# Optimization experiments

Measured on AMD Instinct MI355X. Metric: run time of the kernel, lower is better.

The kernel has to match this reference:

```python
import jax, jax.numpy as jnp
import numpy as np

START_IDX = 1
STOP_IDX = 2
VOCAB = 32000
EMB = 512
HID = 512


def setup_inputs() -> dict:
    key = jax.random.key(0)
    ks = jax.random.split(key, 10)
    B, T = 64, 50
    x = jax.random.normal(ks[0], (B, HID), dtype=jnp.float32)
    labels = jax.random.randint(ks[1], (B, T), 0, VOCAB, dtype=jnp.int64)
    s = 0.02
    emb = jax.random.normal(ks[2], (VOCAB, EMB), dtype=jnp.float32) * s
    W_ih = jax.random.normal(ks[3], (4 * HID, EMB), dtype=jnp.float32) * s
    W_hh = jax.random.normal(ks[4], (4 * HID, HID), dtype=jnp.float32) * s
    b_ih = jax.random.normal(ks[5], (4 * HID,), dtype=jnp.float32) * s
    b_hh = jax.random.normal(ks[6], (4 * HID,), dtype=jnp.float32) * s
    fc_W = jax.random.normal(ks[7], (VOCAB, HID), dtype=jnp.float32) * s
    fc_b = jax.random.normal(ks[8], (VOCAB,), dtype=jnp.float32) * s
    return {"x": x, "labels": labels, "emb": emb, "W_ih": W_ih, "W_hh": W_hh,
            "b_ih": b_ih, "b_hh": b_hh, "fc_W": fc_W, "fc_b": fc_b}


def _decode_loss(x, labels, emb, W_ih, W_hh, b_ih, b_hh, fc_W, fc_b):
    B, T = labels.shape
    # teacher-forced inputs: [START, y_0..y_{T-1}]; targets: [y_0..y_{T-1}, STOP]
    inputs = jnp.concatenate([jnp.full((B, 1), START_IDX, labels.dtype), labels], axis=1)
    targets = jnp.concatenate([labels, jnp.full((B, 1), STOP_IDX, labels.dtype)], axis=1)
    x_emb = emb[inputs]                       # [B, T+1, E]
    x_emb_t = jnp.swapaxes(x_emb, 0, 1)       # [T+1, B, E]

    def step(carry, xt):
        h, c = carry
        gates = xt @ W_ih.T + b_ih + h @ W_hh.T + b_hh   # [B, 4H]
        i, f, g, o = jnp.split(gates, 4, axis=-1)         # torch gate order i,f,g,o
        i = jax.nn.sigmoid(i); f = jax.nn.sigmoid(f)
        g = jnp.tanh(g); o = jax.nn.sigmoid(o)
        c = f * c + i * g
        h = o * jnp.tanh(c)
        return (h, c), h

    # init_states(x[i]): hidden and cell initialized from image feature
    (_, _), hs = jax.lax.scan(step, (x, x), x_emb_t)      # hs: [T+1, B, H]
    logits = hs @ fc_W.T + fc_b                            # [T+1, B, V]
    logp = jax.nn.log_softmax(logits, axis=-1)
    tgt = jnp.swapaxes(targets, 0, 1)[..., None]           # [T+1, B, 1]
    nll = -jnp.take_along_axis(logp, tgt, axis=-1)         # [T+1, B, 1]
    # original: per-step CrossEntropyLoss on batch of 1, summed over steps, / batch_size
    return nll.sum() / B


def reference(x, labels, emb, W_ih, W_hh, b_ih, b_hh, fc_W, fc_b):
    return _decode_loss(x, labels, emb, W_ih, W_hh, b_ih, b_hh, fc_W, fc_b)
```

## Files before the change

### kernel.cpp

```cpp
#include <hip/hip_runtime.h>
#include <cstddef>
#include <cstdint>

#define B_  64
#define T_  51
#define H_  512
#define G4_ 2048
#define V_  32000
#define R_  (T_ * B_)

typedef __attribute__((ext_vector_type(8))) short bf16x8;
typedef __attribute__((ext_vector_type(4))) float f32x4;
typedef __attribute__((ext_vector_type(4))) unsigned int u32x4;
typedef unsigned long long ull;

__device__ __forceinline__ uint16_t f2bf(float f) {
    uint32_t u = __float_as_uint(f);
    u += 0x7FFFu + ((u >> 16) & 1u);
    return (uint16_t)(u >> 16);
}
__device__ __forceinline__ float bf2f(uint32_t h) { return __uint_as_float(h << 16); }

__device__ __forceinline__ void ldsc(u32x4& d, const uint32_t* p) {
    asm volatile("global_load_dwordx4 %0, %1, off sc0 sc1" : "=v"(d) : "v"(p));
}
__device__ __forceinline__ uint32_t ldflag(const uint32_t* p) {
    uint32_t v;
    asm volatile("global_load_dword %0, %1, off sc0 sc1\n\ts_waitcnt vmcnt(0)"
                 : "=v"(v) : "v"(p));
    return v;
}
__device__ __forceinline__ void stflag(uint32_t* p, uint32_t v) {
    asm volatile("global_store_dword %0, %1, off sc0 sc1" :: "v"(p), "v"(v) : "memory");
}
__device__ __forceinline__ void stsh(uint16_t* p, uint32_t v) {
    asm volatile("global_store_short %0, %1, off sc0 sc1" :: "v"(p), "v"(v) : "memory");
}

__device__ __forceinline__ void gl_lds16(const void* g, void* l) {
    __builtin_amdgcn_global_load_lds((const __attribute__((address_space(1))) void*)g,
                                     (__attribute__((address_space(3))) void*)l, 16, 0, 0);
}

__global__ __launch_bounds__(256) void k0_init(const float* __restrict__ x,
                                               uint16_t* __restrict__ hx,
                                               float* __restrict__ sumexp,
                                               uint32_t* __restrict__ flags) {
    int i = blockIdx.x * 256 + threadIdx.x;
    if (i < B_ * H_) hx[i] = f2bf(x[i]);
    if (i < R_) sumexp[i] = 0.f;
    if (i < T_ * 128) flags[i] = 0;
}

__global__ __launch_bounds__(256) void kcvt(const float* __restrict__ src,
                                            uint16_t* __restrict__ dst, int n8) {
    int i = blockIdx.x * 256 + threadIdx.x;
    if (i >= n8) return;
    const float4* s = (const float4*)src + (size_t)i * 2;
    float4 f0 = s[0], f1 = s[1];
    union { uint16_t h[8]; uint4 u; } p;
    p.h[0]=f2bf(f0.x); p.h[1]=f2bf(f0.y); p.h[2]=f2bf(f0.z); p.h[3]=f2bf(f0.w);
    p.h[4]=f2bf(f1.x); p.h[5]=f2bf(f1.y); p.h[6]=f2bf(f1.z); p.h[7]=f2bf(f1.w);
    ((uint4*)dst)[i] = p.u;
}

template<int CVT>
__global__ __launch_bounds__(256, 2) void k1_mfma(const int* __restrict__ labels,
                                                  const float* __restrict__ emb,
                                                  const void* __restrict__ wih,
                                                  const float* __restrict__ b_ih,
                                                  const float* __restrict__ b_hh,
                                                  uint16_t* __restrict__ XgT) {
    __shared__ uint16_t Al[64 * 72];
    __shared__ uint16_t Bl[256 * 72];
    const int t    = blockIdx.y;
    const int n0   = blockIdx.x * 256;
    const int tid  = threadIdx.x;
    const int w    = tid >> 6;
    const int lane = tid & 63;
    const int l15  = lane & 15;
    const int lhi  = lane >> 4;

    f32x4 acc[4][4];
    #pragma unroll
    for (int mi = 0; mi < 4; ++mi)
        #pragma unroll
        for (int nf = 0; nf < 4; ++nf) acc[mi][nf] = (f32x4){0.f, 0.f, 0.f, 0.f};

    for (int k0 = 0; k0 < H_; k0 += 64) {
        #pragma unroll
        for (int r = 0; r < 2; ++r) {
            int idx = r * 256 + tid, row = idx >> 3, seg = idx & 7;
            int tok = (t == 0) ? 1 : labels[row * 50 + (t - 1)];
            const float* s = emb + (size_t)tok * H_ + k0 + seg * 8;
            float4 f0 = *(const float4*)s;
            float4 f1 = *(const float4*)(s + 4);
            union { uint16_t h[8]; uint4 u; } p;
            p.h[0]=f2bf(f0.x); p.h[1]=f2bf(f0.y); p.h[2]=f2bf(f0.z); p.h[3]=f2bf(f0.w);
            p.h[4]=f2bf(f1.x); p.h[5]=f2bf(f1.y); p.h[6]=f2bf(f1.z); p.h[7]=f2bf(f1.w);
            *(uint4*)(Al + row * 72 + seg * 8) = p.u;
        }
        #pragma unroll
        for (int r = 0; r < 8; ++r) {
            int idx = r * 256 + tid, row = idx >> 3, seg = idx & 7;
            if (CVT) {
                const float* s = (const float*)wih + (size_t)(n0 + row) * H_ + k0 + seg * 8;
                float4 f0 = *(const float4*)s;
                float4 f1 = *(const float4*)(s + 4);
                union { uint16_t h[8]; uint4 u; } p;
                p.h[0]=f2bf(f0.x); p.h[1]=f2bf(f0.y); p.h[2]=f2bf(f0.z); p.h[3]=f2bf(f0.w);
                p.h[4]=f2bf(f1.x); p.h[5]=f2bf(f1.y); p.h[6]=f2bf(f1.z); p.h[7]=f2bf(f1.w);
                *(uint4*)(Bl + row * 72 + seg * 8) = p.u;
            } else {
                *(uint4*)(Bl + row * 72 + seg * 8) =
                    *(const uint4*)((const uint16_t*)wih + (size_t)(n0 + row) * H_ + k0 + seg * 8);
            }
        }
        __syncthreads();
        #pragma unroll
        for (int ks = 0; ks < 2; ++ks) {
            bf16x8 a[4];
            #pragma unroll
            for (int mi = 0; mi < 4; ++mi)
                a[mi] = *(const bf16x8*)(Al + (mi * 16 + l15) * 72 + ks * 32 + lhi * 8);
            #pragma unroll
            for (int nf = 0; nf < 4; ++nf) {
                bf16x8 b = *(const bf16x8*)(Bl + (w * 64 + nf * 16 + l15) * 72 + ks * 32 + lhi * 8);
                #pragma unroll
                for (int mi = 0; mi < 4; ++mi)
                    acc[mi][nf] = __builtin_amdgcn_mfma_f32_16x16x32_bf16(a[mi], b, acc[mi][nf], 0, 0, 0);
            }
        }
        __syncthreads();
    }
    float bias[4];
    #pragma unroll
    for (int nf = 0; nf < 4; ++nf) {
        int col = n0 + w * 64 + nf * 16 + l15;
        bias[nf] = b_ih[col] + b_hh[col];
    }
    #pragma unroll
    for (int mi = 0; mi < 4; ++mi)
        #pragma unroll
        for (int nf = 0; nf < 4; ++nf) {
            const int col = n0 + w * 64 + nf * 16 + l15;
            const int g = col >> 9, u = col & 511;
            const int b = mi * 16 + lhi * 4;
            union { uint16_t h[4]; ull q; } pk;
            #pragma unroll
            for (int q = 0; q < 4; ++q) pk.h[q] = f2bf(acc[mi][nf][q] + bias[nf]);
            *(ull*)(XgT + ((size_t)(t * 512 + u) * 4 + g) * 64 + b) = pk.q;
        }
}

__global__ __launch_bounds__(256, 1) void k2p(const uint16_t* __restrict__ hx,
                                              const float* __restrict__ x,
                                              const uint16_t* __restrict__ XgT,
                                              const float* __restrict__ W_hh,
                                              uint16_t* __restrict__ hs,
                                              uint32_t* __restrict__ flags) {
    __shared__ uint16_t Wl[64 * 520];
    const int tid  = threadIdx.x;
    const int bid  = blockIdx.x;
    const int u0   = bid * 16;
    const int w    = tid >> 6;
    const int lane = tid & 63;
    const int l15  = lane & 15;
    const int lhi  = lane >> 4;
    const int arow = w * 16 + l15;

    {
        const int c = tid >> 2;
        const int q = tid & 3;
        const int j = (c >> 4) * 512 + u0 + (c & 15);
        const float* src = W_hh + (size_t)j * H_ + q * 128;
        uint16_t* dst = Wl + c * 520 + q * 128;
        #pragma unroll
        for (int i = 0; i < 128; i += 8) {
            float4 f0 = *(const float4*)(src + i);
            float4 f1 = *(const float4*)(src + i + 4);
            union { uint16_t h[8]; uint4 u; } p;
            p.h[0]=f2bf(f0.x); p.h[1]=f2bf(f0.y); p.h[2]=f2bf(f0.z); p.h[3]=f2bf(f0.w);
            p.h[4]=f2bf(f1.x); p.h[5]=f2bf(f1.y); p.h[6]=f2bf(f1.z); p.h[7]=f2bf(f1.w);
            *(uint4*)(dst + i) = p.u;
        }
    }
    float cst[4];
    #pragma unroll
    for (int q = 0; q < 4; ++q)
        cst[q] = x[(size_t)(w * 16 + lhi * 4 + q) * H_ + u0 + l15];
    __syncthreads();

    for (int t = 0; t < T_; ++t) {
        ull xgp[4];
        #pragma unroll
        for (int g = 0; g < 4; ++g)
            xgp[g] = *(const ull*)(XgT + ((size_t)(t * 512 + u0 + l15) * 4 + g) * 64 + w * 16 + lhi * 4);

        u32x4 ha[16];
        if (t == 0) {
            const uint16_t* hb = hx + (size_t)arow * H_ + lhi * 8;
            #pragma unroll
            for (int ks = 0; ks < 16; ++ks)
                ha[ks] = *(const u32x4*)(hb + ks * 32);
        } else {
            const uint32_t* fp = flags + (size_t)(t - 1) * 128 + (lane & 31) * 4 + w;
            for (;;) {
                uint32_t fv = 1;
                if (lane < 32) fv = ldflag(fp);
                if (!__any((int)(fv == 0))) break;
            }
            __builtin_amdgcn_sched_barrier(0);
            const uint16_t* hb = hs + ((size_t)(t - 1) * 64 + arow) * H_ + lhi * 8;
            #pragma unroll
            for (int ks = 0; ks < 16; ++ks)
                ldsc(ha[ks], (const uint32_t*)(hb + ks * 32));
        }
        f32x4 acc[4];
        #pragma unroll
        for (int nf = 0; nf < 4; ++nf) acc[nf] = (f32x4){0.f, 0.f, 0.f, 0.f};
        if (t != 0) { asm volatile("s_waitcnt vmcnt(8)" ::: "memory");
                      __builtin_amdgcn_sched_barrier(0); }
        #pragma unroll
        for (int ks = 0; ks < 8; ++ks) {
            union { u32x4 u; bf16x8 v; } au; au.u = ha[ks];
            #pragma unroll
            for (int nf = 0; nf < 4; ++nf) {
                bf16x8 b = *(const bf16x8*)(Wl + (nf * 16 + l15) * 520 + ks * 32 + lhi * 8);
                acc[nf] = __builtin_amdgcn_mfma_f32_16x16x32_bf16(au.v, b, acc[nf], 0, 0, 0);
            }
        }
        if (t != 0) { asm volatile("s_waitcnt vmcnt(0)" ::: "memory");
                      __builtin_amdgcn_sched_barrier(0); }
        #pragma unroll
        for (int ks = 8; ks < 16; ++ks) {
            union { u32x4 u; bf16x8 v; } au; au.u = ha[ks];
            #pragma unroll
            for (int nf = 0; nf < 4; ++nf) {
                bf16x8 b = *(const bf16x8*)(Wl + (nf * 16 + l15) * 520 + ks * 32 + lhi * 8);
                acc[nf] = __builtin_amdgcn_mfma_f32_16x16x32_bf16(au.v, b, acc[nf], 0, 0, 0);
            }
        }
        #pragma unroll
        for (int q = 0; q < 4; ++q) {
            const int b = w * 16 + lhi * 4 + q;
            float gi = acc[0][q] + bf2f((uint32_t)((xgp[0] >> (16 * q)) & 0xFFFF));
            float gf = acc[1][q] + bf2f((uint32_t)((xgp[1] >> (16 * q)) & 0xFFFF));
            float gg = acc[2][q] + bf2f((uint32_t)((xgp[2] >> (16 * q)) & 0xFFFF));
            float go = acc[3][q] + bf2f((uint32_t)((xgp[3] >> (16 * q)) & 0xFFFF));
            float si = 1.f / (1.f + __expf(-gi));
            float sf = 1.f / (1.f + __expf(-gf));
            float tg = tanhf(gg);
            float so = 1.f / (1.f + __expf(-go));
            float cc = sf * cst[q] + si * tg;
            cst[q] = cc;
            stsh(hs + (size_t)(t * 64 + b) * H_ + u0 + l15, (uint32_t)f2bf(so * tanhf(cc)));
        }
        asm volatile("s_waitcnt vmcnt(0)" ::: "memory");
        if (lane == 0) stflag(flags + (size_t)t * 128 + bid * 4 + w, (uint32_t)(t + 1));
    }
}

template<int CVT>
__global__ __launch_bounds__(512, 4) void k3_mfma(const uint16_t* __restrict__ hsb,
                                                  const void* __restrict__ fcw,
                                                  const float* __restrict__ fc_b,
                                                  const int* __restrict__ labels,
                                                  float* __restrict__ sumexp,
                                                  float* __restrict__ tgtlog) {
    __shared__ uint16_t Al[128 * 64];
    __shared__ uint16_t Bl[256 * 64];
    const int flat = blockIdx.x;
    const int xcd  = flat & 7;
    const int slot = flat >> 3;
    const int work = (xcd < 2 ? xcd * 407 : 814 + (xcd - 2) * 406) + slot;
    const int m0   = (work % 26) * 128;
    const int v0   = (work / 26) * 256;
    const int tid  = threadIdx.x;
    const int w    = tid >> 6;
    const int lane = tid & 63;
    const int l15  = lane & 15;
    const int lhi  = lane >> 4;
    const int wm   = w >> 2;
    const int wn   = w & 3;

    f32x4 acc[4][4];
    #pragma unroll
    for (int mi = 0; mi < 4; ++mi)
        #pragma unroll
        for (int nf = 0; nf < 4; ++nf) acc[mi][nf] = (f32x4){0.f, 0.f, 0.f, 0.f};

    const int lrow = lane >> 3;
    const int segp = (lane & 7) ^ lrow;

    for (int k0 = 0; k0 < H_; k0 += 64) {
        #pragma unroll
        for (int r = 0; r < 2; ++r) {
            const int g = w * 2 + r, row0 = g * 8;
            int grow = m0 + row0 + lrow; if (grow >= R_) grow = R_ - 1;
            gl_lds16(hsb + (size_t)grow * H_ + k0 + segp * 8, Al + row0 * 64);
        }
        if (CVT == 0) {
            #pragma unroll
            for (int r = 0; r < 4; ++r) {
                const int g = w * 4 + r, row0 = g * 8;
                gl_lds16((const uint16_t*)fcw + (size_t)(v0 + row0 + lrow) * H_ + k0 + segp * 8,
                         Bl + row0 * 64);
            }
        } else {
            #pragma unroll
            for (int r = 0; r < 4; ++r) {
                int idx = r * 512 + tid, row = idx >> 3, seg = idx & 7;
                const float* s = (const float*)fcw + (size_t)(v0 + row) * H_ + k0 + seg * 8;
                float4 f0 = *(const float4*)s;
                float4 f1 = *(const float4*)(s + 4);
                union { uint16_t h[8]; uint4 u; } p;
                p.h[0]=f2bf(f0.x); p.h[1]=f2bf(f0.y); p.h[2]=f2bf(f0.z); p.h[3]=f2bf(f0.w);
                p.h[4]=f2bf(f1.x); p.h[5]=f2bf(f1.y); p.h[6]=f2bf(f1.z); p.h[7]=f2bf(f1.w);
                *(uint4*)(Bl + row * 64 + (seg ^ (row & 7)) * 8) = p.u;
            }
        }
        __syncthreads();
        #pragma unroll
        for (int ks = 0; ks < 2; ++ks) {
            bf16x8 a[4];
            #pragma unroll
            for (int mi = 0; mi < 4; ++mi) {
                const int ar = wm * 64 + mi * 16 + l15;
                a[mi] = *(const bf16x8*)((const char*)Al + ar * 128 +
                        ((ks * 64 + lhi * 16) ^ ((ar & 7) << 4)));
            }
            #pragma unroll
            for (int nf = 0; nf < 4; ++nf) {
                const int br = wn * 64 + nf * 16 + l15;
                bf16x8 b = *(const bf16x8*)((const char*)Bl + br * 128 +
                           ((ks * 64 + lhi * 16) ^ ((br & 7) << 4)));
                #pragma unroll
                for (int mi = 0; mi < 4; ++mi)
                    acc[mi][nf] = __builtin_amdgcn_mfma_f32_16x16x32_bf16(a[mi], b, acc[mi][nf], 0, 0, 0);
            }
        }
        __syncthreads();
    }
    float bias[4];
    #pragma unroll
    for (int nf = 0; nf < 4; ++nf) bias[nf] = fc_b[v0 + wn * 64 + nf * 16 + l15];
    #pragma unroll
    for (int mi = 0; mi < 4; ++mi) {
        #pragma unroll
        for (int q = 0; q < 4; ++q) {
            const int r = m0 + wm * 64 + mi * 16 + lhi * 4 + q;
            if (r >= R_) continue;
            const int t = r >> 6, b = r & 63;
            const int tgt = (t < 50) ? labels[b * 50 + t] : 2;
            float lsum = 0.f;
            #pragma unroll
            for (int nf = 0; nf < 4; ++nf) {
                const int v = v0 + wn * 64 + nf * 16 + l15;
                float lg = acc[mi][nf][q] + bias[nf];
                lsum += __expf(lg);
                if (v == tgt) tgtlog[r] = lg;
            }
            lsum += __shfl_xor(lsum, 1, 16);
            lsum += __shfl_xor(lsum, 2, 16);
            lsum += __shfl_xor(lsum, 4, 16);
            lsum += __shfl_xor(lsum, 8, 16);
            if (l15 == 0) atomicAdd(&sumexp[r], lsum);
        }
    }
}

__global__ __launch_bounds__(256) void k4_loss(const float* __restrict__ sumexp,
                                               const float* __restrict__ tgtlog,
                                               float* __restrict__ out) {
    __shared__ float red[256];
    float s = 0.f;
    for (int r = threadIdx.x; r < R_; r += 256) s += logf(sumexp[r]) - tgtlog[r];
    red[threadIdx.x] = s;
    __syncthreads();
    for (int st = 128; st > 0; st >>= 1) {
        if (threadIdx.x < st) red[threadIdx.x] += red[threadIdx.x + st];
        __syncthreads();
    }
    if (threadIdx.x == 0) out[0] = red[0] / 64.0f;
}

extern "C" void kernel_launch(void* const* d_in, const int* in_sizes, int n_in,
                              void* d_out, int out_size, void* d_ws, size_t ws_size,
                              hipStream_t stream) {
    const float* x      = (const float*)d_in[0];
    const int*   labels = (const int*)d_in[1];
    const float* emb    = (const float*)d_in[2];
    const float* W_ih   = (const float*)d_in[3];
    const float* W_hh   = (const float*)d_in[4];
    const float* b_ih   = (const float*)d_in[5];
    const float* b_hh   = (const float*)d_in[6];
    const float* fc_W   = (const float*)d_in[7];
    const float* fc_b   = (const float*)d_in[8];
    float* out = (float*)d_out;

    char* p = (char*)d_ws;
    uint16_t* XgT    = (uint16_t*)p;  p += (size_t)T_ * 512 * 4 * 64 * 2;
    uint16_t* hsb    = (uint16_t*)p;  p += (size_t)R_ * H_ * 2;
    uint16_t* hx     = (uint16_t*)p;  p += (size_t)B_ * H_ * 2;
    float*    sumexp = (float*)p;     p += (size_t)R_ * 4;
    float*    tgtl   = (float*)p;     p += (size_t)R_ * 4;
    uint32_t* flags  = (uint32_t*)p;  p += (size_t)T_ * 128 * 4 + 256;
    uint16_t* fcwb   = (uint16_t*)p;  p += (size_t)V_ * H_ * 2;
    uint16_t* wihb   = (uint16_t*)p;  p += (size_t)G4_ * H_ * 2;
    const bool pre = ((size_t)(p - (char*)d_ws) <= ws_size);

    k0_init<<<128, 256, 0, stream>>>(x, hx, sumexp, flags);
    if (pre) {
        kcvt<<<8000, 256, 0, stream>>>(fc_W, fcwb, (V_ * H_) / 8);
        kcvt<<<512, 256, 0, stream>>>(W_ih, wihb, (G4_ * H_) / 8);
        k1_mfma<0><<<dim3(8, 51), 256, 0, stream>>>(labels, emb, wihb, b_ih, b_hh, XgT);
    } else {
        k1_mfma<1><<<dim3(8, 51), 256, 0, stream>>>(labels, emb, W_ih, b_ih, b_hh, XgT);
    }
    k2p<<<32, 256, 0, stream>>>(hx, x, XgT, W_hh, hsb, flags);
    if (pre) k3_mfma<0><<<3250, 512, 0, stream>>>(hsb, fcwb, fc_b, labels, sumexp, tgtl);
    else     k3_mfma<1><<<3250, 512, 0, stream>>>(hsb, fc_W, fc_b, labels, sumexp, tgtl);
    k4_loss<<<1, 256, 0, stream>>>(sumexp, tgtl, out);
}
```

Before: 508.3 us.

## Fuse LSTM recurrence and vocab projection into one persistent kernel with flag-based overlap

Merges the recurrent kernel and the vocabulary-projection/softmax kernel into one launch of 256 blocks. The first 32 blocks run the LSTM recurrence while the other 224 blocks loop over 128x256 output tiles, each spinning on per-timestep flags until the hidden states it needs exist. The point is to overlap the latency-bound serial recurrence with the large projection GEMM. In exchange the GEMM path drops the async global-to-LDS loads and the XOR swizzle in favour of register-staged padded LDS with atomic loads, and its grid shrinks from 3250 blocks of 512 threads to 224 persistent blocks of 256 threads. This may cut GEMM throughput, and correctness depends on all blocks being co-resident.

```diff
diff --git a/kernel.cpp b/kernel.cpp
--- a/kernel.cpp
+++ b/kernel.cpp
@@ -8,6 +8,8 @@
 #define G4_ 2048
 #define V_  32000
 #define R_  (T_ * B_)
+#define NTILE 3250
+#define NFC   224
 
 typedef __attribute__((ext_vector_type(8))) short bf16x8;
 typedef __attribute__((ext_vector_type(4))) float f32x4;
@@ -35,11 +37,6 @@
 }
 __device__ __forceinline__ void stsh(uint16_t* p, uint32_t v) {
     asm volatile("global_store_short %0, %1, off sc0 sc1" :: "v"(p), "v"(v) : "memory");
-}
-
-__device__ __forceinline__ void gl_lds16(const void* g, void* l) {
-    __builtin_amdgcn_global_load_lds((const __attribute__((address_space(1))) void*)g,
-                                     (__attribute__((address_space(3))) void*)l, 16, 0, 0);
 }
 
 __global__ __launch_bounds__(256) void k0_init(const float* __restrict__ x,
@@ -153,220 +150,216 @@
         }
 }
 
-__global__ __launch_bounds__(256, 1) void k2p(const uint16_t* __restrict__ hx,
-                                              const float* __restrict__ x,
-                                              const uint16_t* __restrict__ XgT,
-                                              const float* __restrict__ W_hh,
-                                              uint16_t* __restrict__ hs,
-                                              uint32_t* __restrict__ flags) {
-    __shared__ uint16_t Wl[64 * 520];
-    const int tid  = threadIdx.x;
+template<int CVT>
+__global__ __launch_bounds__(256) void k23(const uint16_t* __restrict__ hx,
+                                           const float* __restrict__ x,
+                                           const uint16_t* __restrict__ XgT,
+                                           const float* __restrict__ W_hh,
+                                           uint16_t* __restrict__ hs,
+                                           uint32_t* __restrict__ flags,
+                                           const void* __restrict__ fcw,
+                                           const float* __restrict__ fc_b,
+                                           const int* __restrict__ labels,
+                                           float* __restrict__ sumexp,
+                                           float* __restrict__ tgtlog) {
+    __shared__ uint16_t smem[64 * 520];
     const int bid  = blockIdx.x;
-    const int u0   = bid * 16;
-    const int w    = tid >> 6;
-    const int lane = tid & 63;
-    const int l15  = lane & 15;
-    const int lhi  = lane >> 4;
-    const int arow = w * 16 + l15;
-
-    {
-        const int c = tid >> 2;
-        const int q = tid & 3;
-        const int j = (c >> 4) * 512 + u0 + (c & 15);
-        const float* src = W_hh + (size_t)j * H_ + q * 128;
-        uint16_t* dst = Wl + c * 520 + q * 128;
-        #pragma unroll
-        for (int i = 0; i < 128; i += 8) {
-            float4 f0 = *(const float4*)(src + i);
-            float4 f1 = *(const float4*)(src + i + 4);
-            union { uint16_t h[8]; uint4 u; } p;
-            p.h[0]=f2bf(f0.x); p.h[1]=f2bf(f0.y); p.h[2]=f2bf(f0.z); p.h[3]=f2bf(f0.w);
-            p.h[4]=f2bf(f1.x); p.h[5]=f2bf(f1.y); p.h[6]=f2bf(f1.z); p.h[7]=f2bf(f1.w);
-            *(uint4*)(dst + i) = p.u;
-        }
-    }
-    float cst[4];
-    #pragma unroll
-    for (int q = 0; q < 4; ++q)
-        cst[q] = x[(size_t)(w * 16 + lhi * 4 + q) * H_ + u0 + l15];
-    __syncthreads();
-
-    for (int t = 0; t < T_; ++t) {
-        ull xgp[4];
-        #pragma unroll
-        for (int g = 0; g < 4; ++g)
-            xgp[g] = *(const ull*)(XgT + ((size_t)(t * 512 + u0 + l15) * 4 + g) * 64 + w * 16 + lhi * 4);
-
-        u32x4 ha[16];
-        if (t == 0) {
-            const uint16_t* hb = hx + (size_t)arow * H_ + lhi * 8;
-            #pragma unroll
-            for (int ks = 0; ks < 16; ++ks)
-                ha[ks] = *(const u32x4*)(hb + ks * 32);
-        } else {
-            const uint32_t* fp = flags + (size_t)(t - 1) * 128 + (lane & 31) * 4 + w;
-            for (;;) {
-                uint32_t fv = 1;
-                if (lane < 32) fv = ldflag(fp);
-                if (!__any((int)(fv == 0))) break;
-            }
-            __builtin_amdgcn_sched_barrier(0);
-            const uint16_t* hb = hs + ((size_t)(t - 1) * 64 + arow) * H_ + lhi * 8;
-            #pragma unroll
-            for (int ks = 0; ks < 16; ++ks)
-                ldsc(ha[ks], (const uint32_t*)(hb + ks * 32));
-        }
-        f32x4 acc[4];
-        #pragma unroll
-        for (int nf = 0; nf < 4; ++nf) acc[nf] = (f32x4){0.f, 0.f, 0.f, 0.f};
-        if (t != 0) { asm volatile("s_waitcnt vmcnt(8)" ::: "memory");
-                      __builtin_amdgcn_sched_barrier(0); }
-        #pragma unroll
-        for (int ks = 0; ks < 8; ++ks) {
-            union { u32x4 u; bf16x8 v; } au; au.u = ha[ks];
-            #pragma unroll
-            for (int nf = 0; nf < 4; ++nf) {
-                bf16x8 b = *(const bf16x8*)(Wl + (nf * 16 + l15) * 520 + ks * 32 + lhi * 8);
-                acc[nf] = __builtin_amdgcn_mfma_f32_16x16x32_bf16(au.v, b, acc[nf], 0, 0, 0);
-            }
-        }
-        if (t != 0) { asm volatile("s_waitcnt vmcnt(0)" ::: "memory");
-                      __builtin_amdgcn_sched_barrier(0); }
-        #pragma unroll
-        for (int ks = 8; ks < 16; ++ks) {
-            union { u32x4 u; bf16x8 v; } au; au.u = ha[ks];
-            #pragma unroll
-            for (int nf = 0; nf < 4; ++nf) {
-                bf16x8 b = *(const bf16x8*)(Wl + (nf * 16 + l15) * 520 + ks * 32 + lhi * 8);
-                acc[nf] = __builtin_amdgcn_mfma_f32_16x16x32_bf16(au.v, b, acc[nf], 0, 0, 0);
-            }
-        }
-        #pragma unroll
-        for (int q = 0; q < 4; ++q) {
-            const int b = w * 16 + lhi * 4 + q;
-            float gi = acc[0][q] + bf2f((uint32_t)((xgp[0] >> (16 * q)) & 0xFFFF));
-            float gf = acc[1][q] + bf2f((uint32_t)((xgp[1] >> (16 * q)) & 0xFFFF));
-            float gg = acc[2][q] + bf2f((uint32_t)((xgp[2] >> (16 * q)) & 0xFFFF));
-            float go = acc[3][q] + bf2f((uint32_t)((xgp[3] >> (16 * q)) & 0xFFFF));
-            float si = 1.f / (1.f + __expf(-gi));
-            float sf = 1.f / (1.f + __expf(-gf));
-            float tg = tanhf(gg);
-            float so = 1.f / (1.f + __expf(-go));
-            float cc = sf * cst[q] + si * tg;
-            cst[q] = cc;
-            stsh(hs + (size_t)(t * 64 + b) * H_ + u0 + l15, (uint32_t)f2bf(so * tanhf(cc)));
-        }
-        asm volatile("s_waitcnt vmcnt(0)" ::: "memory");
-        if (lane == 0) stflag(flags + (size_t)t * 128 + bid * 4 + w, (uint32_t)(t + 1));
-    }
-}
-
-template<int CVT>
-__global__ __launch_bounds__(512, 4) void k3_mfma(const uint16_t* __restrict__ hsb,
-                                                  const void* __restrict__ fcw,
-                                                  const float* __restrict__ fc_b,
-                                                  const int* __restrict__ labels,
-                                                  float* __restrict__ sumexp,
-                                                  float* __restrict__ tgtlog) {
-    __shared__ uint16_t Al[128 * 64];
-    __shared__ uint16_t Bl[256 * 64];
-    const int flat = blockIdx.x;
-    const int xcd  = flat & 7;
-    const int slot = flat >> 3;
-    const int work = (xcd < 2 ? xcd * 407 : 814 + (xcd - 2) * 406) + slot;
-    const int m0   = (work % 26) * 128;
-    const int v0   = (work / 26) * 256;
     const int tid  = threadIdx.x;
     const int w    = tid >> 6;
     const int lane = tid & 63;
     const int l15  = lane & 15;
     const int lhi  = lane >> 4;
-    const int wm   = w >> 2;
-    const int wn   = w & 3;
-
-    f32x4 acc[4][4];
-    #pragma unroll
-    for (int mi = 0; mi < 4; ++mi)
-        #pragma unroll
-        for (int nf = 0; nf < 4; ++nf) acc[mi][nf] = (f32x4){0.f, 0.f, 0.f, 0.f};
-
-    const int lrow = lane >> 3;
-    const int segp = (lane & 7) ^ lrow;
-
-    for (int k0 = 0; k0 < H_; k0 += 64) {
-        #pragma unroll
-        for (int r = 0; r < 2; ++r) {
-            const int g = w * 2 + r, row0 = g * 8;
-            int grow = m0 + row0 + lrow; if (grow >= R_) grow = R_ - 1;
-            gl_lds16(hsb + (size_t)grow * H_ + k0 + segp * 8, Al + row0 * 64);
-        }
-        if (CVT == 0) {
-            #pragma unroll
-            for (int r = 0; r < 4; ++r) {
-                const int g = w * 4 + r, row0 = g * 8;
-                gl_lds16((const uint16_t*)fcw + (size_t)(v0 + row0 + lrow) * H_ + k0 + segp * 8,
-                         Bl + row0 * 64);
-            }
-        } else {
-            #pragma unroll
-            for (int r = 0; r < 4; ++r) {
-                int idx = r * 512 + tid, row = idx >> 3, seg = idx & 7;
-                const float* s = (const float*)fcw + (size_t)(v0 + row) * H_ + k0 + seg * 8;
-                float4 f0 = *(const float4*)s;
-                float4 f1 = *(const float4*)(s + 4);
+
+    if (bid < 32) {
+        uint16_t* Wl = smem;
+        const int u0   = bid * 16;
+        const int arow = w * 16 + l15;
+        {
+            const int c = tid >> 2;
+            const int q = tid & 3;
+            const int j = (c >> 4) * 512 + u0 + (c & 15);
+            const float* src = W_hh + (size_t)j * H_ + q * 128;
+            uint16_t* dst = Wl + c * 520 + q * 128;
+            #pragma unroll
+            for (int i = 0; i < 128; i += 8) {
+                float4 f0 = *(const float4*)(src + i);
+                float4 f1 = *(const float4*)(src + i + 4);
                 union { uint16_t h[8]; uint4 u; } p;
                 p.h[0]=f2bf(f0.x); p.h[1]=f2bf(f0.y); p.h[2]=f2bf(f0.z); p.h[3]=f2bf(f0.w);
                 p.h[4]=f2bf(f1.x); p.h[5]=f2bf(f1.y); p.h[6]=f2bf(f1.z); p.h[7]=f2bf(f1.w);
-                *(uint4*)(Bl + row * 64 + (seg ^ (row & 7)) * 8) = p.u;
-            }
-        }
-        __syncthreads();
-        #pragma unroll
-        for (int ks = 0; ks < 2; ++ks) {
-            bf16x8 a[4];
-            #pragma unroll
-            for (int mi = 0; mi < 4; ++mi) {
-                const int ar = wm * 64 + mi * 16 + l15;
-                a[mi] = *(const bf16x8*)((const char*)Al + ar * 128 +
-                        ((ks * 64 + lhi * 16) ^ ((ar & 7) << 4)));
-            }
-            #pragma unroll
-            for (int nf = 0; nf < 4; ++nf) {
-                const int br = wn * 64 + nf * 16 + l15;
-                bf16x8 b = *(const bf16x8*)((const char*)Bl + br * 128 +
-                           ((ks * 64 + lhi * 16) ^ ((br & 7) << 4)));
-                #pragma unroll
-                for (int mi = 0; mi < 4; ++mi)
-                    acc[mi][nf] = __builtin_amdgcn_mfma_f32_16x16x32_bf16(a[mi], b, acc[mi][nf], 0, 0, 0);
-            }
-        }
-        __syncthreads();
-    }
-    float bias[4];
-    #pragma unroll
-    for (int nf = 0; nf < 4; ++nf) bias[nf] = fc_b[v0 + wn * 64 + nf * 16 + l15];
-    #pragma unroll
-    for (int mi = 0; mi < 4; ++mi) {
-        #pragma unroll
-        for (int q = 0; q < 4; ++q) {
-            const int r = m0 + wm * 64 + mi * 16 + lhi * 4 + q;
-            if (r >= R_) continue;
-            const int t = r >> 6, b = r & 63;
-            const int tgt = (t < 50) ? labels[b * 50 + t] : 2;
-            float lsum = 0.f;
-            #pragma unroll
-            for (int nf = 0; nf < 4; ++nf) {
-                const int v = v0 + wn * 64 + nf * 16 + l15;
-                float lg = acc[mi][nf][q] + bias[nf];
-                lsum += __expf(lg);
-                if (v == tgt) tgtlog[r] = lg;
-            }
-            lsum += __shfl_xor(lsum, 1, 16);
-            lsum += __shfl_xor(lsum, 2, 16);
-            lsum += __shfl_xor(lsum, 4, 16);
-            lsum += __shfl_xor(lsum, 8, 16);
-            if (l15 == 0) atomicAdd(&sumexp[r], lsum);
-        }
+                *(uint4*)(dst + i) = p.u;
+            }
+        }
+        float cst[4];
+        #pragma unroll
+        for (int q = 0; q < 4; ++q)
+            cst[q] = x[(size_t)(w * 16 + lhi * 4 + q) * H_ + u0 + l15];
+        __syncthreads();
+
+        for (int t = 0; t < T_; ++t) {
+            ull xgp[4];
+            #pragma unroll
+            for (int g = 0; g < 4; ++g)
+                xgp[g] = *(const ull*)(XgT + ((size_t)(t * 512 + u0 + l15) * 4 + g) * 64 + w * 16 + lhi * 4);
+
+            u32x4 ha[16];
+            if (t == 0) {
+                const uint16_t* hb = hx + (size_t)arow * H_ + lhi * 8;
+                #pragma unroll
+                for (int ks = 0; ks < 16; ++ks)
+                    ha[ks] = *(const u32x4*)(hb + ks * 32);
+            } else {
+                const uint32_t* fp = flags + (size_t)(t - 1) * 128 + (lane & 31) * 4 + w;
+                for (;;) {
+                    uint32_t fv = 1;
+                    if (lane < 32) fv = ldflag(fp);
+                    if (!__any((int)(fv == 0))) break;
+                }
+                __builtin_amdgcn_sched_barrier(0);
+                const uint16_t* hb = hs + ((size_t)(t - 1) * 64 + arow) * H_ + lhi * 8;
+                #pragma unroll
+                for (int ks = 0; ks < 16; ++ks)
+                    ldsc(ha[ks], (const uint32_t*)(hb + ks * 32));
+            }
+            f32x4 acc[4];
+            #pragma unroll
+            for (int nf = 0; nf < 4; ++nf) acc[nf] = (f32x4){0.f, 0.f, 0.f, 0.f};
+            if (t != 0) { asm volatile("s_waitcnt vmcnt(8)" ::: "memory");
+                          __builtin_amdgcn_sched_barrier(0); }
+            #pragma unroll
+            for (int ks = 0; ks < 8; ++ks) {
+                union { u32x4 u; bf16x8 v; } au; au.u = ha[ks];
+                #pragma unroll
+                for (int nf = 0; nf < 4; ++nf) {
+                    bf16x8 b = *(const bf16x8*)(Wl + (nf * 16 + l15) * 520 + ks * 32 + lhi * 8);
+                    acc[nf] = __builtin_amdgcn_mfma_f32_16x16x32_bf16(au.v, b, acc[nf], 0, 0, 0);
+                }
+            }
+            if (t != 0) { asm volatile("s_waitcnt vmcnt(0)" ::: "memory");
+                          __builtin_amdgcn_sched_barrier(0); }
+            #pragma unroll
+            for (int ks = 8; ks < 16; ++ks) {
+                union { u32x4 u; bf16x8 v; } au; au.u = ha[ks];
+                #pragma unroll
+                for (int nf = 0; nf < 4; ++nf) {
+                    bf16x8 b = *(const bf16x8*)(Wl + (nf * 16 + l15) * 520 + ks * 32 + lhi * 8);
+                    acc[nf] = __builtin_amdgcn_mfma_f32_16x16x32_bf16(au.v, b, acc[nf], 0, 0, 0);
+                }
+            }
+            #pragma unroll
+            for (int q = 0; q < 4; ++q) {
+                const int b = w * 16 + lhi * 4 + q;
+                float gi = acc[0][q] + bf2f((uint32_t)((xgp[0] >> (16 * q)) & 0xFFFF));
+                float gf = acc[1][q] + bf2f((uint32_t)((xgp[1] >> (16 * q)) & 0xFFFF));
+                float gg = acc[2][q] + bf2f((uint32_t)((xgp[2] >> (16 * q)) & 0xFFFF));
+                float go = acc[3][q] + bf2f((uint32_t)((xgp[3] >> (16 * q)) & 0xFFFF));
+                float si = 1.f / (1.f + __expf(-gi));
+                float sf = 1.f / (1.f + __expf(-gf));
+                float tg = tanhf(gg);
+                float so = 1.f / (1.f + __expf(-go));
+                float cc = sf * cst[q] + si * tg;
+                cst[q] = cc;
+                stsh(hs + (size_t)(t * 64 + b) * H_ + u0 + l15, (uint32_t)f2bf(so * tanhf(cc)));
+            }
+            asm volatile("s_waitcnt vmcnt(0)" ::: "memory");
+            if (lane == 0) stflag(flags + (size_t)t * 128 + bid * 4 + w, (uint32_t)(t + 1));
+        }
+        return;
+    }
+
+    uint16_t* Al = smem;
+    uint16_t* Bl = smem + 128 * 72;
+    int ready_t = -1;
+    for (int id = bid - 32; id < NTILE; id += NFC) {
+        const int m0 = (id / 125) * 128;
+        const int v0 = (id % 125) * 256;
+        const int mt = (m0 + 127) >> 6;
+        const int maxt = mt > 50 ? 50 : mt;
+        if (maxt > ready_t) {
+            if (tid < 128)
+                while (ldflag(flags + (size_t)maxt * 128 + tid) == 0)
+                    __builtin_amdgcn_s_sleep(8);
+            ready_t = maxt;
+        }
+        __syncthreads();
+
+        f32x4 acc[8][4];
+        #pragma unroll
+        for (int mi = 0; mi < 8; ++mi)
+            #pragma unroll
+            for (int nf = 0; nf < 4; ++nf) acc[mi][nf] = (f32x4){0.f, 0.f, 0.f, 0.f};
+
+        for (int k0 = 0; k0 < H_; k0 += 64) {
+            #pragma unroll
+            for (int r = 0; r < 4; ++r) {
+                int idx = r * 256 + tid, row = idx >> 3, seg = idx & 7;
+                int grow = m0 + row; if (grow >= R_) grow = R_ - 1;
+                const ull* p = (const ull*)(hs + (size_t)grow * H_ + k0 + seg * 8);
+                union { ull q[2]; uint4 u; } d;
+                d.q[0] = __hip_atomic_load(p,     __ATOMIC_RELAXED, __HIP_MEMORY_SCOPE_AGENT);
+                d.q[1] = __hip_atomic_load(p + 1, __ATOMIC_RELAXED, __HIP_MEMORY_SCOPE_AGENT);
+                *(uint4*)(Al + row * 72 + seg * 8) = d.u;
+            }
+            #pragma unroll
+            for (int r = 0; r < 8; ++r) {
+                int idx = r * 256 + tid, row = idx >> 3, seg = idx & 7;
+                if (CVT) {
+                    const float* s = (const float*)fcw + (size_t)(v0 + row) * H_ + k0 + seg * 8;
+                    float4 f0 = *(const float4*)s;
+                    float4 f1 = *(const float4*)(s + 4);
+                    union { uint16_t h[8]; uint4 u; } p;
+                    p.h[0]=f2bf(f0.x); p.h[1]=f2bf(f0.y); p.h[2]=f2bf(f0.z); p.h[3]=f2bf(f0.w);
+                    p.h[4]=f2bf(f1.x); p.h[5]=f2bf(f1.y); p.h[6]=f2bf(f1.z); p.h[7]=f2bf(f1.w);
+                    *(uint4*)(Bl + row * 72 + seg * 8) = p.u;
+                } else {
+                    *(uint4*)(Bl + row * 72 + seg * 8) =
+                        *(const uint4*)((const uint16_t*)fcw + (size_t)(v0 + row) * H_ + k0 + seg * 8);
+                }
+            }
+            __syncthreads();
+            #pragma unroll
+            for (int ks = 0; ks < 2; ++ks) {
+                bf16x8 a[8];
+                #pragma unroll
+                for (int mi = 0; mi < 8; ++mi)
+                    a[mi] = *(const bf16x8*)(Al + (mi * 16 + l15) * 72 + ks * 32 + lhi * 8);
+                #pragma unroll
+                for (int nf = 0; nf < 4; ++nf) {
+                    bf16x8 b = *(const bf16x8*)(Bl + (w * 64 + nf * 16 + l15) * 72 + ks * 32 + lhi * 8);
+                    #pragma unroll
+                    for (int mi = 0; mi < 8; ++mi)
+                        acc[mi][nf] = __builtin_amdgcn_mfma_f32_16x16x32_bf16(a[mi], b, acc[mi][nf], 0, 0, 0);
+                }
+            }
+            __syncthreads();
+        }
+        float bias[4];
+        #pragma unroll
+        for (int nf = 0; nf < 4; ++nf) bias[nf] = fc_b[v0 + w * 64 + nf * 16 + l15];
+        #pragma unroll
+        for (int mi = 0; mi < 8; ++mi) {
+            #pragma unroll
+            for (int q = 0; q < 4; ++q) {
+                const int r = m0 + mi * 16 + lhi * 4 + q;
+                if (r >= R_) continue;
+                const int t = r >> 6, b = r & 63;
+                const int tgt = (t < 50) ? labels[b * 50 + t] : 2;
+                float lsum = 0.f;
+                #pragma unroll
+                for (int nf = 0; nf < 4; ++nf) {
+                    const int v = v0 + w * 64 + nf * 16 + l15;
+                    float lg = acc[mi][nf][q] + bias[nf];
+                    lsum += __expf(lg);
+                    if (v == tgt) tgtlog[r] = lg;
+                }
+                lsum += __shfl_xor(lsum, 1, 16);
+                lsum += __shfl_xor(lsum, 2, 16);
+                lsum += __shfl_xor(lsum, 4, 16);
+                lsum += __shfl_xor(lsum, 8, 16);
+                if (l15 == 0) atomicAdd(&sumexp[r], lsum);
+            }
+        }
+        __syncthreads();
     }
 }
 
@@ -415,11 +408,12 @@
         kcvt<<<8000, 256, 0, stream>>>(fc_W, fcwb, (V_ * H_) / 8);
         kcvt<<<512, 256, 0, stream>>>(W_ih, wihb, (G4_ * H_) / 8);
         k1_mfma<0><<<dim3(8, 51), 256, 0, stream>>>(labels, emb, wihb, b_ih, b_hh, XgT);
+        k23<0><<<256, 256, 0, stream>>>(hx, x, XgT, W_hh, hsb, flags,
+                                        fcwb, fc_b, labels, sumexp, tgtl);
     } else {
         k1_mfma<1><<<dim3(8, 51), 256, 0, stream>>>(labels, emb, W_ih, b_ih, b_hh, XgT);
-    }
-    k2p<<<32, 256, 0, stream>>>(hx, x, XgT, W_hh, hsb, flags);
-    if (pre) k3_mfma<0><<<3250, 512, 0, stream>>>(hsb, fcwb, fc_b, labels, sumexp, tgtl);
-    else     k3_mfma<1><<<3250, 512, 0, stream>>>(hsb, fc_W, fc_b, labels, sumexp, tgtl);
+        k23<1><<<256, 256, 0, stream>>>(hx, x, XgT, W_hh, hsb, flags,
+                                        fc_W, fc_b, labels, sumexp, tgtl);
+    }
     k4_loss<<<1, 256, 0, stream>>>(sumexp, tgtl, out);
 }
```

New measurement: 699.1 us. 1.38x slower.

## Swap MFMA operands in LSTM recurrence, vectorize h stores, split flag wait

Applied to the files above, without the earlier changes.

The recurrent kernel now puts W_hh in the A operand and h in the B operand, so each lane's accumulator holds four consecutive hidden units of one batch row. This lets h be written with a single 8-byte store instead of four 2-byte stores, and lets the cell state load as one float4. The precomputed input-gate buffer switches to a row-major [row, 4H] layout to match, which turns the k1 epilogue into scattered 2-byte stores. The flag wait is split in two: the first half of the previous h is loaded once its producer blocks are ready, and the second half is waited for separately, so part of the load overlaps the remaining wait.

```diff
diff --git a/kernel.cpp b/kernel.cpp
--- a/kernel.cpp
+++ b/kernel.cpp
@@ -33,8 +33,8 @@
 __device__ __forceinline__ void stflag(uint32_t* p, uint32_t v) {
     asm volatile("global_store_dword %0, %1, off sc0 sc1" :: "v"(p), "v"(v) : "memory");
 }
-__device__ __forceinline__ void stsh(uint16_t* p, uint32_t v) {
-    asm volatile("global_store_short %0, %1, off sc0 sc1" :: "v"(p), "v"(v) : "memory");
+__device__ __forceinline__ void stq(uint16_t* p, ull v) {
+    asm volatile("global_store_dwordx2 %0, %1, off sc0 sc1" :: "v"(p), "v"(v) : "memory");
 }
 
 __device__ __forceinline__ void gl_lds16(const void* g, void* l) {
@@ -70,7 +70,7 @@
                                                   const void* __restrict__ wih,
                                                   const float* __restrict__ b_ih,
                                                   const float* __restrict__ b_hh,
-                                                  uint16_t* __restrict__ XgT) {
+                                                  uint16_t* __restrict__ Xg) {
     __shared__ uint16_t Al[64 * 72];
     __shared__ uint16_t Bl[256 * 72];
     const int t    = blockIdx.y;
@@ -144,18 +144,17 @@
         #pragma unroll
         for (int nf = 0; nf < 4; ++nf) {
             const int col = n0 + w * 64 + nf * 16 + l15;
-            const int g = col >> 9, u = col & 511;
-            const int b = mi * 16 + lhi * 4;
-            union { uint16_t h[4]; ull q; } pk;
-            #pragma unroll
-            for (int q = 0; q < 4; ++q) pk.h[q] = f2bf(acc[mi][nf][q] + bias[nf]);
-            *(ull*)(XgT + ((size_t)(t * 512 + u) * 4 + g) * 64 + b) = pk.q;
+            #pragma unroll
+            for (int q = 0; q < 4; ++q) {
+                const int r = t * 64 + mi * 16 + lhi * 4 + q;
+                Xg[(size_t)r * G4_ + col] = f2bf(acc[mi][nf][q] + bias[nf]);
+            }
         }
 }
 
 __global__ __launch_bounds__(256, 1) void k2p(const uint16_t* __restrict__ hx,
                                               const float* __restrict__ x,
-                                              const uint16_t* __restrict__ XgT,
+                                              const uint16_t* __restrict__ Xg,
                                               const float* __restrict__ W_hh,
                                               uint16_t* __restrict__ hs,
                                               uint32_t* __restrict__ flags) {
@@ -185,17 +184,14 @@
             *(uint4*)(dst + i) = p.u;
         }
     }
-    float cst[4];
-    #pragma unroll
-    for (int q = 0; q < 4; ++q)
-        cst[q] = x[(size_t)(w * 16 + lhi * 4 + q) * H_ + u0 + l15];
+    float4 cst = *(const float4*)(x + (size_t)arow * H_ + u0 + lhi * 4);
     __syncthreads();
 
     for (int t = 0; t < T_; ++t) {
         ull xgp[4];
         #pragma unroll
         for (int g = 0; g < 4; ++g)
-            xgp[g] = *(const ull*)(XgT + ((size_t)(t * 512 + u0 + l15) * 4 + g) * 64 + w * 16 + lhi * 4);
+            xgp[g] = *(const ull*)(Xg + (size_t)(t * 64 + arow) * G4_ + g * 512 + u0 + lhi * 4);
 
         u32x4 ha[16];
         if (t == 0) {
@@ -204,46 +200,56 @@
             for (int ks = 0; ks < 16; ++ks)
                 ha[ks] = *(const u32x4*)(hb + ks * 32);
         } else {
-            const uint32_t* fp = flags + (size_t)(t - 1) * 128 + (lane & 31) * 4 + w;
+            const uint16_t* hb = hs + ((size_t)(t - 1) * 64 + arow) * H_ + lhi * 8;
+            const uint32_t* fpl = flags + (size_t)(t - 1) * 128 + (lane & 15) * 4 + w;
             for (;;) {
                 uint32_t fv = 1;
-                if (lane < 32) fv = ldflag(fp);
+                if (lane < 16) fv = ldflag(fpl);
                 if (!__any((int)(fv == 0))) break;
             }
             __builtin_amdgcn_sched_barrier(0);
-            const uint16_t* hb = hs + ((size_t)(t - 1) * 64 + arow) * H_ + lhi * 8;
-            #pragma unroll
-            for (int ks = 0; ks < 16; ++ks)
+            #pragma unroll
+            for (int ks = 0; ks < 8; ++ks)
                 ldsc(ha[ks], (const uint32_t*)(hb + ks * 32));
+            const uint32_t* fph = flags + (size_t)(t - 1) * 128 + (16 + (lane & 15)) * 4 + w;
+            for (;;) {
+                uint32_t fv = 1;
+                if (lane < 16) fv = ldflag(fph);
+                if (!__any((int)(fv == 0))) break;
+            }
+            __builtin_amdgcn_sched_barrier(0);
+            #pragma unroll
+            for (int ks = 8; ks < 16; ++ks)
+                ldsc(ha[ks], (const uint32_t*)(hb + ks * 32));
         }
         f32x4 acc[4];
         #pragma unroll
-        for (int nf = 0; nf < 4; ++nf) acc[nf] = (f32x4){0.f, 0.f, 0.f, 0.f};
+        for (int g = 0; g < 4; ++g) acc[g] = (f32x4){0.f, 0.f, 0.f, 0.f};
         if (t != 0) { asm volatile("s_waitcnt vmcnt(8)" ::: "memory");
                       __builtin_amdgcn_sched_barrier(0); }
         #pragma unroll
         for (int ks = 0; ks < 8; ++ks) {
-            union { u32x4 u; bf16x8 v; } au; au.u = ha[ks];
-            #pragma unroll
-            for (int nf = 0; nf < 4; ++nf) {
-                bf16x8 b = *(const bf16x8*)(Wl + (nf * 16 + l15) * 520 + ks * 32 + lhi * 8);
-                acc[nf] = __builtin_amdgcn_mfma_f32_16x16x32_bf16(au.v, b, acc[nf], 0, 0, 0);
+            union { u32x4 u; bf16x8 v; } bu; bu.u = ha[ks];
+            #pragma unroll
+            for (int g = 0; g < 4; ++g) {
+                bf16x8 a = *(const bf16x8*)(Wl + (g * 16 + l15) * 520 + ks * 32 + lhi * 8);
+                acc[g] = __builtin_amdgcn_mfma_f32_16x16x32_bf16(a, bu.v, acc[g], 0, 0, 0);
             }
         }
         if (t != 0) { asm volatile("s_waitcnt vmcnt(0)" ::: "memory");
                       __builtin_amdgcn_sched_barrier(0); }
         #pragma unroll
         for (int ks = 8; ks < 16; ++ks) {
-            union { u32x4 u; bf16x8 v; } au; au.u = ha[ks];
-            #pragma unroll
-            for (int nf = 0; nf < 4; ++nf) {
-                bf16x8 b = *(const bf16x8*)(Wl + (nf * 16 + l15) * 520 + ks * 32 + lhi * 8);
-                acc[nf] = __builtin_amdgcn_mfma_f32_16x16x32_bf16(au.v, b, acc[nf], 0, 0, 0);
-            }
-        }
+            union { u32x4 u; bf16x8 v; } bu; bu.u = ha[ks];
+            #pragma unroll
+            for (int g = 0; g < 4; ++g) {
+                bf16x8 a = *(const bf16x8*)(Wl + (g * 16 + l15) * 520 + ks * 32 + lhi * 8);
+                acc[g] = __builtin_amdgcn_mfma_f32_16x16x32_bf16(a, bu.v, acc[g], 0, 0, 0);
+            }
+        }
+        union { uint16_t h[4]; ull q8; } hv;
         #pragma unroll
         for (int q = 0; q < 4; ++q) {
-            const int b = w * 16 + lhi * 4 + q;
             float gi = acc[0][q] + bf2f((uint32_t)((xgp[0] >> (16 * q)) & 0xFFFF));
             float gf = acc[1][q] + bf2f((uint32_t)((xgp[1] >> (16 * q)) & 0xFFFF));
             float gg = acc[2][q] + bf2f((uint32_t)((xgp[2] >> (16 * q)) & 0xFFFF));
@@ -254,8 +260,9 @@
             float so = 1.f / (1.f + __expf(-go));
             float cc = sf * cst[q] + si * tg;
             cst[q] = cc;
-            stsh(hs + (size_t)(t * 64 + b) * H_ + u0 + l15, (uint32_t)f2bf(so * tanhf(cc)));
-        }
+            hv.h[q] = f2bf(so * tanhf(cc));
+        }
+        stq(hs + (size_t)(t * 64 + arow) * H_ + u0 + lhi * 4, hv.q8);
         asm volatile("s_waitcnt vmcnt(0)" ::: "memory");
         if (lane == 0) stflag(flags + (size_t)t * 128 + bid * 4 + w, (uint32_t)(t + 1));
     }
@@ -400,7 +407,7 @@
     float* out = (float*)d_out;
 
     char* p = (char*)d_ws;
-    uint16_t* XgT    = (uint16_t*)p;  p += (size_t)T_ * 512 * 4 * 64 * 2;
+    uint16_t* Xg     = (uint16_t*)p;  p += (size_t)R_ * G4_ * 2;
     uint16_t* hsb    = (uint16_t*)p;  p += (size_t)R_ * H_ * 2;
     uint16_t* hx     = (uint16_t*)p;  p += (size_t)B_ * H_ * 2;
     float*    sumexp = (float*)p;     p += (size_t)R_ * 4;
@@ -414,11 +421,11 @@
     if (pre) {
         kcvt<<<8000, 256, 0, stream>>>(fc_W, fcwb, (V_ * H_) / 8);
         kcvt<<<512, 256, 0, stream>>>(W_ih, wihb, (G4_ * H_) / 8);
-        k1_mfma<0><<<dim3(8, 51), 256, 0, stream>>>(labels, emb, wihb, b_ih, b_hh, XgT);
+        k1_mfma<0><<<dim3(8, 51), 256, 0, stream>>>(labels, emb, wihb, b_ih, b_hh, Xg);
     } else {
-        k1_mfma<1><<<dim3(8, 51), 256, 0, stream>>>(labels, emb, W_ih, b_ih, b_hh, XgT);
-    }
-    k2p<<<32, 256, 0, stream>>>(hx, x, XgT, W_hh, hsb, flags);
+        k1_mfma<1><<<dim3(8, 51), 256, 0, stream>>>(labels, emb, W_ih, b_ih, b_hh, Xg);
+    }
+    k2p<<<32, 256, 0, stream>>>(hx, x, Xg, W_hh, hsb, flags);
     if (pre) k3_mfma<0><<<3250, 512, 0, stream>>>(hsb, fcwb, fc_b, labels, sumexp, tgtl);
     else     k3_mfma<1><<<3250, 512, 0, stream>>>(hsb, fc_W, fc_b, labels, sumexp, tgtl);
     k4_loss<<<1, 256, 0, stream>>>(sumexp, tgtl, out);
```

Result: slower. 546.9 us (+7.6%).
